# Optimization experiments

Measured on AMD Instinct MI355X. Metric: run time of the kernel, lower is better.

## Reference

```python
import jax, jax.numpy as jnp
import numpy as np

B, S, D_MODEL = 2, 2048, 1024
NUM_HEADS = 16
D_HEAD = D_MODEL // NUM_HEADS
THETA = 10000.0


def setup_inputs() -> dict:
    key = jax.random.key(0)
    ks = jax.random.split(key, 5)
    std = float(np.sqrt(2.0 / (D_MODEL + D_MODEL)))
    return {
        "x": jax.random.normal(ks[0], (B, S, D_MODEL), dtype=jnp.float32),
        "wq": jax.random.normal(ks[1], (D_MODEL, D_MODEL), dtype=jnp.float32) * std,
        "wk": jax.random.normal(ks[2], (D_MODEL, D_MODEL), dtype=jnp.float32) * std,
        "wv": jax.random.normal(ks[3], (D_MODEL, D_MODEL), dtype=jnp.float32) * std,
        "wo": jax.random.normal(ks[4], (D_MODEL, D_MODEL), dtype=jnp.float32) * std,
    }


def _apply_rope(x):
    # x: [b, h, s, d]; interleaved even/odd RoPE rotation
    d = x.shape[-1]
    s = x.shape[-2]
    inv_freq = 1.0 / (THETA ** (jnp.arange(0, d, 2, dtype=x.dtype) / d))  # [d/2]
    pos = jnp.arange(s, dtype=x.dtype)
    freqs = pos[:, None] * inv_freq[None, :]  # [s, d/2]
    cos, sin = jnp.cos(freqs), jnp.sin(freqs)
    x_even = x[..., 0::2]
    x_odd = x[..., 1::2]
    rot_even = x_even * cos - x_odd * sin
    rot_odd = x_even * sin + x_odd * cos
    # interleave back: stack pairs on a new trailing axis then flatten
    return jnp.stack([rot_even, rot_odd], axis=-1).reshape(x.shape)


def reference(x, wq, wk, wv, wo):
    b, s, _ = x.shape
    # Linear applies weight [d_out, d_in] as x @ W^T
    q = jnp.einsum('bsd,ed->bse', x, wq)
    k = jnp.einsum('bsd,ed->bse', x, wk)
    v = jnp.einsum('bsd,ed->bse', x, wv)
    # [b, s, h*dh] -> [b, h, s, dh]
    q = q.reshape(b, s, NUM_HEADS, D_HEAD).transpose(0, 2, 1, 3)
    k = k.reshape(b, s, NUM_HEADS, D_HEAD).transpose(0, 2, 1, 3)
    v = v.reshape(b, s, NUM_HEADS, D_HEAD).transpose(0, 2, 1, 3)
    q = _apply_rope(q)
    k = _apply_rope(k)
    scores = jnp.einsum('bhqd,bhkd->bhqk', q, k) / jnp.sqrt(jnp.asarray(D_HEAD, x.dtype))
    causal = jnp.tril(jnp.ones((s, s), dtype=bool))  # allowed positions
    scores = jnp.where(causal, scores, -jnp.inf)
    attn = jax.nn.softmax(scores, axis=-1)
    out = jnp.einsum('bhqk,bhkd->bhqd', attn, v)
    out = out.transpose(0, 2, 1, 3).reshape(b, s, NUM_HEADS * D_HEAD)
    return jnp.einsum('bsd,ed->bse', out, wo)
```

## Files before the change

kernel.cpp:

```cpp
#include <hip/hip_runtime.h>
#include <stdint.h>

typedef unsigned short u16;
typedef __attribute__((ext_vector_type(8))) short bf16x8;
typedef __attribute__((ext_vector_type(4))) short bf16x4;
typedef __attribute__((ext_vector_type(4))) float f32x4;
typedef __attribute__((ext_vector_type(4))) unsigned short u16x4;

#define S_ 2048
#define E_ 1024

__device__ __forceinline__ u16 f2bf(float f) {
  union { float f; unsigned u; } v; v.f = f;
  unsigned u = v.u;
  unsigned r = (u + 0x7FFFu + ((u >> 16) & 1u)) >> 16;
  return (u16)r;
}
__device__ __forceinline__ float bf2f(u16 h) {
  union { unsigned u; float f; } v; v.u = ((unsigned)h) << 16;
  return v.f;
}

typedef __attribute__((address_space(3))) void lds_void;
__device__ __forceinline__ unsigned lds_off(void* p) {
  return (unsigned)(unsigned long long)(lds_void*)p;
}
__device__ __forceinline__ void glds16(const u16* g, u16* l) {
  __builtin_amdgcn_global_load_lds(
      (const __attribute__((address_space(1))) void*)g,
      (__attribute__((address_space(3))) void*)l, 16, 0, 0);
}

__global__ void k_cast5(const float* __restrict__ x,
                        const float* __restrict__ wq, const float* __restrict__ wk,
                        const float* __restrict__ wv, const float* __restrict__ wo,
                        u16* __restrict__ xb, u16* __restrict__ wqb, u16* __restrict__ wkb,
                        u16* __restrict__ wvb, u16* __restrict__ wob) {
  int i = blockIdx.x * blockDim.x + threadIdx.x;
  const float* src; u16* dst; int off;
  if (i < 1048576) { src = x; dst = xb; off = i; }
  else {
    int j = i - 1048576;
    int w = j >> 18; off = j & 262143;
    src = (w == 0) ? wq : (w == 1) ? wk : (w == 2) ? wv : wo;
    dst = (w == 0) ? wqb : (w == 1) ? wkb : (w == 2) ? wvb : wob;
  }
  float4 v = *((const float4*)src + off);
  u16x4 o;
  o.x = f2bf(v.x); o.y = f2bf(v.y); o.z = f2bf(v.z); o.w = f2bf(v.w);
  *((u16x4*)dst + off) = o;
}

__global__ __launch_bounds__(256) void k_gemm(
    const u16* __restrict__ A,
    const u16* __restrict__ W0, const u16* __restrict__ W1, const u16* __restrict__ W2,
    void* O0, void* O1, void* O2, int outF32)
{
  __shared__ __align__(16) u16 As[2][128 * 32];
  __shared__ __align__(16) u16 Ws[2][128 * 32];
  int tid = threadIdx.x;
  int wid = tid >> 6, lane = tid & 63;
  int lg = lane >> 4, lr = lane & 15;
  int wsel = blockIdx.y >> 3, nb = blockIdx.y & 7;
  const u16* W = (wsel == 0) ? W0 : ((wsel == 1) ? W1 : W2);
  void* O = (wsel == 0) ? O0 : ((wsel == 1) ? O1 : O2);
  int m0 = blockIdx.x * 128;
  int n0 = nb * 128;
  int wr = wid >> 1, wc = wid & 1;

  f32x4 acc[4][4];
#pragma unroll
  for (int m = 0; m < 4; m++)
#pragma unroll
    for (int n = 0; n < 4; n++) acc[m][n] = (f32x4){0.f, 0.f, 0.f, 0.f};

  int srow = tid >> 2;
  int schunk = (tid & 3) ^ ((tid >> 3) & 3);
  const u16* ag = A + (size_t)(m0 + srow) * 1024 + schunk * 8;
  const u16* wg = W + (size_t)(n0 + srow) * 1024 + schunk * 8;

  int buf = 0;
  glds16(ag, &As[0][tid * 8]);
  glds16(ag + 65536, &As[0][tid * 8 + 2048]);
  glds16(wg, &Ws[0][tid * 8]);
  glds16(wg + 65536, &Ws[0][tid * 8 + 2048]);
  __syncthreads();

  for (int kt = 0; kt < 1024; kt += 32) {
    if (kt + 32 < 1024) {
      glds16(ag + kt + 32, &As[buf ^ 1][tid * 8]);
      glds16(ag + kt + 32 + 65536, &As[buf ^ 1][tid * 8 + 2048]);
      glds16(wg + kt + 32, &Ws[buf ^ 1][tid * 8]);
      glds16(wg + kt + 32 + 65536, &Ws[buf ^ 1][tid * 8 + 2048]);
    }
    bf16x8 af[4], wf[4];
#pragma unroll
    for (int m = 0; m < 4; m++) {
      int row = wr * 64 + m * 16 + lr;
      af[m] = *(const bf16x8*)&As[buf][row * 32 + ((lg ^ ((row >> 1) & 3)) * 8)];
    }
#pragma unroll
    for (int n = 0; n < 4; n++) {
      int row = wc * 64 + n * 16 + lr;
      wf[n] = *(const bf16x8*)&Ws[buf][row * 32 + ((lg ^ ((row >> 1) & 3)) * 8)];
    }
    __builtin_amdgcn_s_setprio(1);
#pragma unroll
    for (int m = 0; m < 4; m++)
#pragma unroll
      for (int n = 0; n < 4; n++)
        acc[m][n] = __builtin_amdgcn_mfma_f32_16x16x32_bf16(af[m], wf[n], acc[m][n], 0, 0, 0);
    __builtin_amdgcn_s_setprio(0);
    __syncthreads();
    buf ^= 1;
  }

#pragma unroll
  for (int m = 0; m < 4; m++) {
    int gr = m0 + wr * 64 + m * 16 + lg * 4;
#pragma unroll
    for (int n = 0; n < 4; n++) {
      int gc = n0 + wc * 64 + n * 16 + lr;
#pragma unroll
      for (int r = 0; r < 4; r++) {
        if (outF32) ((float*)O)[(size_t)(gr + r) * 1024 + gc] = acc[m][n][r];
        else ((u16*)O)[(size_t)(gr + r) * 1024 + gc] = f2bf(acc[m][n][r]);
      }
    }
  }
}

__global__ void k_rope(u16* __restrict__ Q, u16* __restrict__ K) {
  int idx = blockIdx.x * blockDim.x + threadIdx.x;
  int p = idx & 511;
  int srow = idx >> 9;
  int s = srow & (S_ - 1);
  int i = p & 31;
  float ang = (float)s * exp2f(-0.415241012f * (float)i);
  float sn, c;
  __sincosf(ang, &sn, &c);
  unsigned* qp = (unsigned*)Q + idx;
  unsigned qv = *qp;
  float e = bf2f((u16)(qv & 0xffff)), o = bf2f((u16)(qv >> 16));
  float re = e * c - o * sn, ro = e * sn + o * c;
  *qp = (unsigned)f2bf(re) | ((unsigned)f2bf(ro) << 16);
  unsigned* kp = (unsigned*)K + idx;
  unsigned kv = *kp;
  e = bf2f((u16)(kv & 0xffff)); o = bf2f((u16)(kv >> 16));
  re = e * c - o * sn; ro = e * sn + o * c;
  *kp = (unsigned)f2bf(re) | ((unsigned)f2bf(ro) << 16);
}

__global__ __launch_bounds__(256) void k_attn(
    const u16* __restrict__ Q, const u16* __restrict__ K,
    const u16* __restrict__ V, u16* __restrict__ AO)
{
  __shared__ __align__(16) u16 Ks[64 * 64];
  __shared__ __align__(16) u16 Vs[64 * 64];
  int tid = threadIdx.x;
  int wid = tid >> 6, lane = tid & 63;
  int lg = lane >> 4, lr = lane & 15;
  int bh = blockIdx.x;
  int qb = 31 - (int)blockIdx.y;
  int q0 = qb * 64 + wid * 16;
  size_t base = (size_t)(bh >> 4) * (2048u * 1024u) + (size_t)(bh & 15) * 64;

  const u16* qrow = Q + base + (size_t)(q0 + lr) * 1024 + lg * 8;
  bf16x8 qf0 = *(const bf16x8*)(qrow);
  bf16x8 qf1 = *(const bf16x8*)(qrow + 32);

  int srow = tid >> 3;
  int sch = tid & 7;
  const u16* kg = K + base + (size_t)srow * 1024 + sch * 8;
  const u16* vg = V + base + (size_t)srow * 1024 + sch * 8;
  int kwb0 = ((srow)*128 + sch * 16) ^ ((srow & 7) << 4);
  int kwb1 = ((srow + 32) * 128 + sch * 16) ^ ((srow & 7) << 4);
  int vwi0 = (srow >> 4) * 1024 + (sch >> 1) * 256 + (srow & 15) * 16 + (sch & 1) * 8;
  int vwi1 = ((srow + 32) >> 4) * 1024 + (sch >> 1) * 256 + (srow & 15) * 16 + (sch & 1) * 8;

  bf16x8 kr0 = *(const bf16x8*)(kg);
  bf16x8 kr1 = *(const bf16x8*)(kg + 32 * 1024);
  bf16x8 vr0 = *(const bf16x8*)(vg);
  bf16x8 vr1 = *(const bf16x8*)(vg + 32 * 1024);

  float m = -1e30f, lsum = 0.f;
  f32x4 o[4];
#pragma unroll
  for (int c = 0; c < 4; c++) o[c] = (f32x4){0.f, 0.f, 0.f, 0.f};

  int qg = q0 + lr;
  int ntile = qb + 1;
  unsigned vrd = lds_off(Vs) + (unsigned)(lane * 8);

  for (int t = 0; t < ntile; ++t) {
    __syncthreads();
    *(bf16x8*)((char*)Ks + kwb0) = kr0;
    *(bf16x8*)((char*)Ks + kwb1) = kr1;
    *(bf16x8*)(&Vs[vwi0]) = vr0;
    *(bf16x8*)(&Vs[vwi1]) = vr1;
    __syncthreads();
    if (t + 1 < ntile) {
      const u16* kg2 = kg + (size_t)(t + 1) * 64 * 1024;
      const u16* vg2 = vg + (size_t)(t + 1) * 64 * 1024;
      kr0 = *(const bf16x8*)(kg2);
      kr1 = *(const bf16x8*)(kg2 + 32 * 1024);
      vr0 = *(const bf16x8*)(vg2);
      vr1 = *(const bf16x8*)(vg2 + 32 * 1024);
    }
    f32x4 sv[4];
    int kv0 = t * 64;
    __builtin_amdgcn_s_setprio(1);
#pragma unroll
    for (int sub = 0; sub < 4; ++sub) {
      int row = sub * 16 + lr;
      int swz = (row & 7) << 4;
      bf16x8 kf0 = *(const bf16x8*)((const char*)Ks + ((row * 128 + lg * 16) ^ swz));
      bf16x8 kf1 = *(const bf16x8*)((const char*)Ks + ((row * 128 + 64 + lg * 16) ^ swz));
      f32x4 z = (f32x4){0.f, 0.f, 0.f, 0.f};
      z = __builtin_amdgcn_mfma_f32_16x16x32_bf16(kf0, qf0, z, 0, 0, 0);
      sv[sub] = __builtin_amdgcn_mfma_f32_16x16x32_bf16(kf1, qf1, z, 0, 0, 0);
    }
    __builtin_amdgcn_s_setprio(0);
    if (t == ntile - 1) {
#pragma unroll
      for (int sub = 0; sub < 4; ++sub)
#pragma unroll
        for (int j = 0; j < 4; ++j) {
          int kvg = kv0 + sub * 16 + lg * 4 + j;
          sv[sub][j] = (kvg <= qg) ? sv[sub][j] * 0.125f : -1e30f;
        }
    } else {
#pragma unroll
      for (int sub = 0; sub < 4; ++sub)
#pragma unroll
        for (int j = 0; j < 4; ++j) sv[sub][j] *= 0.125f;
    }
    float tm = -1e30f;
#pragma unroll
    for (int sub = 0; sub < 4; ++sub)
#pragma unroll
      for (int j = 0; j < 4; ++j) tm = fmaxf(tm, sv[sub][j]);
    tm = fmaxf(tm, __shfl_xor(tm, 16));
    tm = fmaxf(tm, __shfl_xor(tm, 32));
    float mn = fmaxf(m, tm);
    float corr = __expf(m - mn);
    m = mn;
    lsum *= corr;
#pragma unroll
    for (int c = 0; c < 4; ++c) {
      o[c][0] *= corr; o[c][1] *= corr; o[c][2] *= corr; o[c][3] *= corr;
    }
    bf16x4 pb[4];
#pragma unroll
    for (int sub = 0; sub < 4; ++sub)
#pragma unroll
      for (int j = 0; j < 4; ++j) {
        float p = __expf(sv[sub][j] - mn);
        lsum += p;
        pb[sub][j] = (short)f2bf(p);
      }
#pragma unroll
    for (int sub = 0; sub < 4; ++sub) {
      unsigned wa = vrd + (unsigned)(sub * 2048);
      bf16x4 va0, va1, va2, va3;
      asm volatile("ds_read_b64_tr_b16 %0, %1" : "=v"(va0) : "v"(wa));
      asm volatile("ds_read_b64_tr_b16 %0, %1 offset:512" : "=v"(va1) : "v"(wa));
      asm volatile("ds_read_b64_tr_b16 %0, %1 offset:1024" : "=v"(va2) : "v"(wa));
      asm volatile("ds_read_b64_tr_b16 %0, %1 offset:1536" : "=v"(va3) : "v"(wa));
      asm volatile("s_waitcnt lgkmcnt(0)" ::: "memory");
      __builtin_amdgcn_sched_barrier(0);
      __builtin_amdgcn_s_setprio(1);
      o[0] = __builtin_amdgcn_mfma_f32_16x16x16bf16_1k(va0, pb[sub], o[0], 0, 0, 0);
      o[1] = __builtin_amdgcn_mfma_f32_16x16x16bf16_1k(va1, pb[sub], o[1], 0, 0, 0);
      o[2] = __builtin_amdgcn_mfma_f32_16x16x16bf16_1k(va2, pb[sub], o[2], 0, 0, 0);
      o[3] = __builtin_amdgcn_mfma_f32_16x16x16bf16_1k(va3, pb[sub], o[3], 0, 0, 0);
      __builtin_amdgcn_s_setprio(0);
    }
  }

  float lt = lsum + __shfl_xor(lsum, 16);
  lt += __shfl_xor(lt, 32);
  float inv = 1.0f / lt;
  u16* orow = AO + base + (size_t)(q0 + lr) * 1024;
#pragma unroll
  for (int c = 0; c < 4; c++)
#pragma unroll
    for (int r = 0; r < 4; r++)
      orow[c * 16 + lg * 4 + r] = f2bf(o[c][r] * inv);
}

extern "C" void kernel_launch(void* const* d_in, const int* in_sizes, int n_in,
                              void* d_out, int out_size, void* d_ws, size_t ws_size,
                              hipStream_t stream) {
  const float* x = (const float*)d_in[0];
  const float* wq = (const float*)d_in[1];
  const float* wk = (const float*)d_in[2];
  const float* wv = (const float*)d_in[3];
  const float* wo = (const float*)d_in[4];

  char* ws = (char*)d_ws;
  u16* xb  = (u16*)(ws);
  u16* wqb = (u16*)(ws + 8388608);
  u16* wkb = (u16*)(ws + 10485760);
  u16* wvb = (u16*)(ws + 12582912);
  u16* wob = (u16*)(ws + 14680064);
  u16* Qb  = (u16*)(ws + 16777216);
  u16* Kb  = (u16*)(ws + 25165824);
  u16* Vb  = (u16*)(ws + 33554432);
  u16* AO  = (u16*)(ws + 41943040);

  k_cast5<<<8192, 256, 0, stream>>>(x, wq, wk, wv, wo, xb, wqb, wkb, wvb, wob);
  k_gemm<<<dim3(32, 24), 256, 0, stream>>>(xb, wqb, wkb, wvb, Qb, Kb, Vb, 0);
  k_rope<<<8192, 256, 0, stream>>>(Qb, Kb);
  k_attn<<<dim3(32, 32), 256, 0, stream>>>(Qb, Kb, Vb, AO);
  k_gemm<<<dim3(32, 8), 256, 0, stream>>>(AO, wob, wob, wob, d_out, d_out, d_out, 1);
}
```

Before: 120.0 us.

## Fold softmax scale into Q, use exp2, lazy rescale, packed bf16 conversions

Folds the 1/sqrt(d)·log2(e) factor into Q during RoPE so the attention loop uses exp2 with no per-score scaling. Skips the running-max rescale of the output accumulators unless the new max exceeds the old by more than a threshold. Replaces the software bf16 rounding with the hardware packed conversion instruction and vectorizes the output stores. Also hoists the K/V pointer increments and reshapes the max reduction as a tree. The lazy rescale allows exponent values up to 2^8 before correction, which is safe in fp32 but slightly changes the numerics.

```diff
diff --git a/kernel.cpp b/kernel.cpp
--- a/kernel.cpp
+++ b/kernel.cpp
@@ -6,9 +6,11 @@
 typedef __attribute__((ext_vector_type(4))) short bf16x4;
 typedef __attribute__((ext_vector_type(4))) float f32x4;
 typedef __attribute__((ext_vector_type(4))) unsigned short u16x4;
+typedef __attribute__((ext_vector_type(2))) unsigned u32x2;
 
 #define S_ 2048
 #define E_ 1024
+#define QSCALE 0.18033688011112042f
 
 __device__ __forceinline__ u16 f2bf(float f) {
   union { float f; unsigned u; } v; v.f = f;
@@ -19,6 +21,17 @@
 __device__ __forceinline__ float bf2f(u16 h) {
   union { unsigned u; float f; } v; v.u = ((unsigned)h) << 16;
   return v.f;
+}
+__device__ __forceinline__ unsigned cvtpk(float a, float b) {
+  unsigned r;
+  asm("v_cvt_pk_bf16_f32 %0, %1, %2" : "=v"(r) : "v"(a), "v"(b));
+  return r;
+}
+__device__ __forceinline__ bf16x4 pk4(float a, float b, float c, float d) {
+  union { u32x2 u; bf16x4 v; } U;
+  U.u[0] = cvtpk(a, b);
+  U.u[1] = cvtpk(c, d);
+  return U.v;
 }
 
 typedef __attribute__((address_space(3))) void lds_void;
@@ -142,13 +155,13 @@
   unsigned* qp = (unsigned*)Q + idx;
   unsigned qv = *qp;
   float e = bf2f((u16)(qv & 0xffff)), o = bf2f((u16)(qv >> 16));
-  float re = e * c - o * sn, ro = e * sn + o * c;
-  *qp = (unsigned)f2bf(re) | ((unsigned)f2bf(ro) << 16);
+  float re = (e * c - o * sn) * QSCALE, ro = (e * sn + o * c) * QSCALE;
+  *qp = cvtpk(re, ro);
   unsigned* kp = (unsigned*)K + idx;
   unsigned kv = *kp;
   e = bf2f((u16)(kv & 0xffff)); o = bf2f((u16)(kv >> 16));
   re = e * c - o * sn; ro = e * sn + o * c;
-  *kp = (unsigned)f2bf(re) | ((unsigned)f2bf(ro) << 16);
+  *kp = cvtpk(re, ro);
 }
 
 __global__ __launch_bounds__(256) void k_attn(
@@ -182,6 +195,8 @@
   bf16x8 kr1 = *(const bf16x8*)(kg + 32 * 1024);
   bf16x8 vr0 = *(const bf16x8*)(vg);
   bf16x8 vr1 = *(const bf16x8*)(vg + 32 * 1024);
+  const u16* kgp = kg + 64 * 1024;
+  const u16* vgp = vg + 64 * 1024;
 
   float m = -1e30f, lsum = 0.f;
   f32x4 o[4];
@@ -200,12 +215,12 @@
     *(bf16x8*)(&Vs[vwi1]) = vr1;
     __syncthreads();
     if (t + 1 < ntile) {
-      const u16* kg2 = kg + (size_t)(t + 1) * 64 * 1024;
-      const u16* vg2 = vg + (size_t)(t + 1) * 64 * 1024;
-      kr0 = *(const bf16x8*)(kg2);
-      kr1 = *(const bf16x8*)(kg2 + 32 * 1024);
-      vr0 = *(const bf16x8*)(vg2);
-      vr1 = *(const bf16x8*)(vg2 + 32 * 1024);
+      kr0 = *(const bf16x8*)(kgp);
+      kr1 = *(const bf16x8*)(kgp + 32 * 1024);
+      vr0 = *(const bf16x8*)(vgp);
+      vr1 = *(const bf16x8*)(vgp + 32 * 1024);
+      kgp += 64 * 1024;
+      vgp += 64 * 1024;
     }
     f32x4 sv[4];
     int kv0 = t * 64;
@@ -227,38 +242,35 @@
 #pragma unroll
         for (int j = 0; j < 4; ++j) {
           int kvg = kv0 + sub * 16 + lg * 4 + j;
-          sv[sub][j] = (kvg <= qg) ? sv[sub][j] * 0.125f : -1e30f;
+          sv[sub][j] = (kvg <= qg) ? sv[sub][j] : -1e30f;
         }
-    } else {
-#pragma unroll
-      for (int sub = 0; sub < 4; ++sub)
-#pragma unroll
-        for (int j = 0; j < 4; ++j) sv[sub][j] *= 0.125f;
-    }
-    float tm = -1e30f;
-#pragma unroll
-    for (int sub = 0; sub < 4; ++sub)
-#pragma unroll
-      for (int j = 0; j < 4; ++j) tm = fmaxf(tm, sv[sub][j]);
+    }
+    float tm = fmaxf(fmaxf(fmaxf(sv[0][0], sv[0][1]), fmaxf(sv[0][2], sv[0][3])),
+                     fmaxf(fmaxf(sv[1][0], sv[1][1]), fmaxf(sv[1][2], sv[1][3])));
+    tm = fmaxf(tm, fmaxf(fmaxf(fmaxf(sv[2][0], sv[2][1]), fmaxf(sv[2][2], sv[2][3])),
+                         fmaxf(fmaxf(sv[3][0], sv[3][1]), fmaxf(sv[3][2], sv[3][3]))));
     tm = fmaxf(tm, __shfl_xor(tm, 16));
     tm = fmaxf(tm, __shfl_xor(tm, 32));
-    float mn = fmaxf(m, tm);
-    float corr = __expf(m - mn);
-    m = mn;
-    lsum *= corr;
-#pragma unroll
-    for (int c = 0; c < 4; ++c) {
-      o[c][0] *= corr; o[c][1] *= corr; o[c][2] *= corr; o[c][3] *= corr;
+    if (!__all(tm <= m + 8.f)) {
+      float mn = fmaxf(m, tm);
+      float corr = __builtin_amdgcn_exp2f(m - mn);
+      m = mn;
+      lsum *= corr;
+#pragma unroll
+      for (int c = 0; c < 4; ++c) {
+        o[c][0] *= corr; o[c][1] *= corr; o[c][2] *= corr; o[c][3] *= corr;
+      }
     }
     bf16x4 pb[4];
 #pragma unroll
-    for (int sub = 0; sub < 4; ++sub)
-#pragma unroll
-      for (int j = 0; j < 4; ++j) {
-        float p = __expf(sv[sub][j] - mn);
-        lsum += p;
-        pb[sub][j] = (short)f2bf(p);
-      }
+    for (int sub = 0; sub < 4; ++sub) {
+      float p0 = __builtin_amdgcn_exp2f(sv[sub][0] - m);
+      float p1 = __builtin_amdgcn_exp2f(sv[sub][1] - m);
+      float p2 = __builtin_amdgcn_exp2f(sv[sub][2] - m);
+      float p3 = __builtin_amdgcn_exp2f(sv[sub][3] - m);
+      lsum += (p0 + p1) + (p2 + p3);
+      pb[sub] = pk4(p0, p1, p2, p3);
+    }
 #pragma unroll
     for (int sub = 0; sub < 4; ++sub) {
       unsigned wa = vrd + (unsigned)(sub * 2048);
@@ -283,10 +295,12 @@
   float inv = 1.0f / lt;
   u16* orow = AO + base + (size_t)(q0 + lr) * 1024;
 #pragma unroll
-  for (int c = 0; c < 4; c++)
-#pragma unroll
-    for (int r = 0; r < 4; r++)
-      orow[c * 16 + lg * 4 + r] = f2bf(o[c][r] * inv);
+  for (int c = 0; c < 4; c++) {
+    u32x2 pk;
+    pk[0] = cvtpk(o[c][0] * inv, o[c][1] * inv);
+    pk[1] = cvtpk(o[c][2] * inv, o[c][3] * inv);
+    *(u32x2*)&orow[c * 16 + lg * 4] = pk;
+  }
 }
 
 extern "C" void kernel_launch(void* const* d_in, const int* in_sizes, int n_in,
```

Measured after the change: 115.7 us. 3.5% less time.
